# Kernel optimization log

Hardware: AMD Instinct MI355X
Metric: run time of the kernel (lower is better)

Reference implementation:

```python
import jax, jax.numpy as jnp
import numpy as np

B, R, N, F = 8, 8, 1024, 256


def setup_inputs() -> dict:
    key = jax.random.key(0)
    k1, k2 = jax.random.split(key)
    inputs = jax.random.normal(k1, (B, R, N, F), dtype=jnp.float32)
    Bs = jax.random.normal(k2, (R, F, F), dtype=jnp.float32) * 0.05
    return {"inputs": inputs, "Bs": Bs}


def reference(inputs, Bs):
    # E_r @ B_r : [B,R,N,F] x [R,F,F] -> [B,R,N,F]
    e = jnp.einsum("brnf,rfg->brng", inputs, Bs)
    # (E_r B_r) @ E_r^T : [B,R,N,F] x [B,R,M,F] -> [B,R,N,M]
    scores = jnp.einsum("brng,brmg->brnm", e, inputs)
    return jax.nn.sigmoid(scores)
```

## Files before the change

### kernel.cpp

```cpp
#include <hip/hip_runtime.h>


typedef float   f32x4 __attribute__((ext_vector_type(4)));
typedef _Float16 f16x8 __attribute__((ext_vector_type(8)));

#define WS_E_OFF   0
#define WS_BST_OFF 16777216
#define WS_e_OFF   17301504

__global__ __launch_bounds__(256) void bl_convert(
    const float* __restrict__ E, const float* __restrict__ Bs,
    _Float16* __restrict__ wsE, _Float16* __restrict__ wsBsT) {
  int bid = blockIdx.x, tid = threadIdx.x;
  if (bid < 8192) {
    int cid = (bid << 8) + tid;
    int br  = cid >> 15;
    int rem = cid & 32767;
    int fc  = rem >> 10;
    int n   = rem & 1023;
    const float* src = E + ((size_t)br << 18) + n * 256 + (fc << 3);
    f32x4 v0 = *(const f32x4*)src;
    f32x4 v1 = *(const f32x4*)(src + 4);
    f16x8 h;
    h[0] = (_Float16)v0[0]; h[1] = (_Float16)v0[1];
    h[2] = (_Float16)v0[2]; h[3] = (_Float16)v0[3];
    h[4] = (_Float16)v1[0]; h[5] = (_Float16)v1[1];
    h[6] = (_Float16)v1[2]; h[7] = (_Float16)v1[3];
    *(f16x8*)(wsE + ((size_t)br << 18) + (fc << 13) + (n << 3)) = h;
  } else {
    int cid = ((bid - 8192) << 8) + tid;
    int r   = cid >> 13;
    int rem = cid & 8191;
    int fc  = rem >> 8;
    int g   = rem & 255;
    const float* src = Bs + (r << 16) + (fc << 3) * 256 + g;
    f16x8 h;
#pragma unroll
    for (int j = 0; j < 8; ++j) h[j] = (_Float16)src[j * 256];
    *(f16x8*)(wsBsT + (r << 16) + (fc << 11) + (g << 3)) = h;
  }
}

__global__ __launch_bounds__(256) void bl_gemm1(
    const _Float16* __restrict__ wsE, const _Float16* __restrict__ wsBsT,
    _Float16* __restrict__ wse) {
  __shared__ _Float16 sA[8192];
  __shared__ _Float16 sB[8192];
  int bid = blockIdx.x;
  int br = bid >> 4;
  int t  = bid & 15;
  int n0 = (t >> 1) << 7;
  int g0 = (t & 1) << 7;
  int r  = br & 7;
  int tid  = threadIdx.x;
  int lane = tid & 63, wave = tid >> 6;
  int wm = wave >> 1, wn = wave & 1;
  int quad = lane >> 4, l16 = lane & 15;

  const _Float16* aG = wsE   + ((size_t)br << 18) + (n0 << 3);
  const _Float16* bG = wsBsT + (r << 16) + (g0 << 3);

  f32x4 acc[4][4] = {};

  for (int kk = 0; kk < 4; ++kk) {
    __syncthreads();
#pragma unroll
    for (int i = 0; i < 4; ++i) {
      int c = (i << 8) + tid;
      int kcl = c >> 7, nl = c & 127;
      *(f16x8*)&sA[c << 3] = *(const f16x8*)(aG + (((kk << 3) + kcl) << 13) + (nl << 3));
    }
#pragma unroll
    for (int i = 0; i < 4; ++i) {
      int c = (i << 8) + tid;
      int kcl = c >> 7, gl = c & 127;
      *(f16x8*)&sB[c << 3] = *(const f16x8*)(bG + (((kk << 3) + kcl) << 11) + (gl << 3));
    }
    __syncthreads();
#pragma unroll
    for (int ks = 0; ks < 2; ++ks) {
      int kc = (ks << 2) + quad;
      f16x8 af[4], bf[4];
#pragma unroll
      for (int rt = 0; rt < 4; ++rt)
        af[rt] = *(const f16x8*)&sA[((kc << 7) + (wm << 6) + (rt << 4) + l16) << 3];
#pragma unroll
      for (int ct = 0; ct < 4; ++ct)
        bf[ct] = *(const f16x8*)&sB[((kc << 7) + (wn << 6) + (ct << 4) + l16) << 3];
#pragma unroll
      for (int rt = 0; rt < 4; ++rt)
#pragma unroll
        for (int ct = 0; ct < 4; ++ct)
          acc[rt][ct] = __builtin_amdgcn_mfma_f32_16x16x32_f16(af[rt], bf[ct], acc[rt][ct], 0, 0, 0);
    }
  }
  _Float16* eB = wse + ((size_t)br << 18);
#pragma unroll
  for (int rt = 0; rt < 4; ++rt) {
#pragma unroll
    for (int ct = 0; ct < 4; ++ct) {
      int g  = g0 + (wn << 6) + (ct << 4) + l16;
      int gc = g >> 3, gj = g & 7;
#pragma unroll
      for (int i = 0; i < 4; ++i) {
        int n = n0 + (wm << 6) + (rt << 4) + (quad << 2) + i;
        eB[(gc << 13) + (n << 3) + gj] = (_Float16)acc[rt][ct][i];
      }
    }
  }
}

__global__ __launch_bounds__(256) void bl_gemm2(
    const _Float16* __restrict__ wse, const _Float16* __restrict__ wsE,
    float* __restrict__ out) {
  __shared__ _Float16 sA[8192];
  __shared__ _Float16 sB[8192];
  int bid = blockIdx.x;
  int br = bid >> 6;
  int t  = bid & 63;
  int n0 = (t >> 3) << 7;
  int m0 = (t & 7) << 7;
  int tid  = threadIdx.x;
  int lane = tid & 63, wave = tid >> 6;
  int wm = wave >> 1, wn = wave & 1;
  int quad = lane >> 4, l16 = lane & 15;

  const _Float16* aG = wse + ((size_t)br << 18) + (n0 << 3);
  const _Float16* bG = wsE + ((size_t)br << 18) + (m0 << 3);

  f32x4 acc[4][4] = {};

  for (int kk = 0; kk < 4; ++kk) {
    __syncthreads();
#pragma unroll
    for (int i = 0; i < 4; ++i) {
      int c = (i << 8) + tid;
      int kcl = c >> 7, nl = c & 127;
      *(f16x8*)&sA[c << 3] = *(const f16x8*)(aG + (((kk << 3) + kcl) << 13) + (nl << 3));
    }
#pragma unroll
    for (int i = 0; i < 4; ++i) {
      int c = (i << 8) + tid;
      int kcl = c >> 7, ml = c & 127;
      *(f16x8*)&sB[c << 3] = *(const f16x8*)(bG + (((kk << 3) + kcl) << 13) + (ml << 3));
    }
    __syncthreads();
#pragma unroll
    for (int ks = 0; ks < 2; ++ks) {
      int kc = (ks << 2) + quad;
      f16x8 af[4], bf[4];
#pragma unroll
      for (int rt = 0; rt < 4; ++rt)
        af[rt] = *(const f16x8*)&sA[((kc << 7) + (wm << 6) + (rt << 4) + l16) << 3];
#pragma unroll
      for (int ct = 0; ct < 4; ++ct)
        bf[ct] = *(const f16x8*)&sB[((kc << 7) + (wn << 6) + (ct << 4) + l16) << 3];
#pragma unroll
      for (int rt = 0; rt < 4; ++rt)
#pragma unroll
        for (int ct = 0; ct < 4; ++ct)
          acc[rt][ct] = __builtin_amdgcn_mfma_f32_16x16x32_f16(af[rt], bf[ct], acc[rt][ct], 0, 0, 0);
    }
  }
  float* oB = out + ((size_t)br << 20);
#pragma unroll
  for (int rt = 0; rt < 4; ++rt) {
#pragma unroll
    for (int ct = 0; ct < 4; ++ct) {
      int m = m0 + (wn << 6) + (ct << 4) + l16;
#pragma unroll
      for (int i = 0; i < 4; ++i) {
        int n = n0 + (wm << 6) + (rt << 4) + (quad << 2) + i;
        float x = acc[rt][ct][i];
        float s = __builtin_amdgcn_rcpf(1.0f + __expf(-x));
        oB[((size_t)n << 10) + m] = s;
      }
    }
  }
}

extern "C" void kernel_launch(void* const* d_in, const int* in_sizes, int n_in,
                              void* d_out, int out_size, void* d_ws, size_t ws_size,
                              hipStream_t stream) {
  const float* E  = (const float*)d_in[0];
  const float* Bs = (const float*)d_in[1];
  _Float16* wsE   = (_Float16*)d_ws + WS_E_OFF;
  _Float16* wsBsT = (_Float16*)d_ws + WS_BST_OFF;
  _Float16* wse   = (_Float16*)d_ws + WS_e_OFF;
  float* out = (float*)d_out;

  bl_convert<<<8448, 256, 0, stream>>>(E, Bs, wsE, wsBsT);
  bl_gemm1<<<1024, 256, 0, stream>>>(wsE, wsBsT, wse);
  bl_gemm2<<<4096, 256, 0, stream>>>(wse, wsE, out);
}
```

Baseline: 392.8 us.

## Stage convert through LDS, use direct global-to-LDS loads, nontemporal sigmoid stores

The convert kernel now transposes tiles through shared memory, so both the fp32 reads and the fp16 writes are coalesced, and the launch uses far fewer, larger blocks. Both GEMM kernels switch their tile staging to global_load_lds builtins, which write straight into LDS without passing through registers. The gemm2 epilogue precomputes a base output pointer, replaces the rcp intrinsic with a true division, and writes the fp32 output with nontemporal stores. The intent is to cut wasted memory traffic and VGPR pressure, at the cost of an exact divide and a dependence on direct-to-LDS load semantics.

```diff
diff --git a/kernel.cpp b/kernel.cpp
--- a/kernel.cpp
+++ b/kernel.cpp
@@ -1,43 +1,74 @@
 #include <hip/hip_runtime.h>
 
 
-typedef float   f32x4 __attribute__((ext_vector_type(4)));
+typedef float    f32x4 __attribute__((ext_vector_type(4)));
 typedef _Float16 f16x8 __attribute__((ext_vector_type(8)));
 
 #define WS_E_OFF   0
 #define WS_BST_OFF 16777216
 #define WS_e_OFF   17301504
 
+typedef __attribute__((address_space(3))) void  lds_void;
+typedef const __attribute__((address_space(1))) void glb_void;
+#define GLOAD16(gp, lp) __builtin_amdgcn_global_load_lds((glb_void*)(gp), (lds_void*)(lp), 16, 0, 0)
+
 __global__ __launch_bounds__(256) void bl_convert(
     const float* __restrict__ E, const float* __restrict__ Bs,
     _Float16* __restrict__ wsE, _Float16* __restrict__ wsBsT) {
-  int bid = blockIdx.x, tid = threadIdx.x;
-  if (bid < 8192) {
-    int cid = (bid << 8) + tid;
-    int br  = cid >> 15;
-    int rem = cid & 32767;
-    int fc  = rem >> 10;
-    int n   = rem & 1023;
-    const float* src = E + ((size_t)br << 18) + n * 256 + (fc << 3);
-    f32x4 v0 = *(const f32x4*)src;
-    f32x4 v1 = *(const f32x4*)(src + 4);
-    f16x8 h;
-    h[0] = (_Float16)v0[0]; h[1] = (_Float16)v0[1];
-    h[2] = (_Float16)v0[2]; h[3] = (_Float16)v0[3];
-    h[4] = (_Float16)v1[0]; h[5] = (_Float16)v1[1];
-    h[6] = (_Float16)v1[2]; h[7] = (_Float16)v1[3];
-    *(f16x8*)(wsE + ((size_t)br << 18) + (fc << 13) + (n << 3)) = h;
+  __shared__ _Float16 s[16640];
+  int bid = blockIdx.x, t = threadIdx.x;
+  if (bid < 1024) {
+    int br = bid >> 4, n0 = (bid & 15) << 6;
+    const float* src = E + ((size_t)br << 18) + ((size_t)n0 << 8);
+#pragma unroll
+    for (int i = 0; i < 8; ++i) {
+      int idx = (i << 8) + t;
+      int n_l = idx >> 5, fc = idx & 31;
+      const float* p = src + (n_l << 8) + (fc << 3);
+      f32x4 v0 = *(const f32x4*)p;
+      f32x4 v1 = *(const f32x4*)(p + 4);
+      f16x8 h;
+      h[0]=(_Float16)v0[0]; h[1]=(_Float16)v0[1]; h[2]=(_Float16)v0[2]; h[3]=(_Float16)v0[3];
+      h[4]=(_Float16)v1[0]; h[5]=(_Float16)v1[1]; h[6]=(_Float16)v1[2]; h[7]=(_Float16)v1[3];
+      *(f16x8*)&s[fc * 520 + (n_l << 3)] = h;
+    }
+    __syncthreads();
+    _Float16* dst = wsE + ((size_t)br << 18) + (n0 << 3);
+#pragma unroll
+    for (int i = 0; i < 8; ++i) {
+      int idx = (i << 8) + t;
+      int fc = idx >> 6, n_l = idx & 63;
+      *(f16x8*)(dst + (fc << 13) + (n_l << 3)) = *(const f16x8*)&s[fc * 520 + (n_l << 3)];
+    }
   } else {
-    int cid = ((bid - 8192) << 8) + tid;
-    int r   = cid >> 13;
-    int rem = cid & 8191;
-    int fc  = rem >> 8;
-    int g   = rem & 255;
-    const float* src = Bs + (r << 16) + (fc << 3) * 256 + g;
-    f16x8 h;
-#pragma unroll
-    for (int j = 0; j < 8; ++j) h[j] = (_Float16)src[j * 256];
-    *(f16x8*)(wsBsT + (r << 16) + (fc << 11) + (g << 3)) = h;
+    int b2 = bid - 1024;
+    int r = b2 >> 2, f0 = (b2 & 3) << 6;
+    const float* src = Bs + (r << 16) + (f0 << 8);
+#pragma unroll
+    for (int i = 0; i < 8; ++i) {
+      int idx = (i << 8) + t;
+      int f_l = idx >> 5, gc8 = idx & 31;
+      const float* p = src + (f_l << 8) + (gc8 << 3);
+      f32x4 v0 = *(const f32x4*)p;
+      f32x4 v1 = *(const f32x4*)(p + 4);
+      int base = (f_l >> 3) * 2056 + (gc8 << 6) + (f_l & 7);
+      s[base +  0] = (_Float16)v0[0];
+      s[base +  8] = (_Float16)v0[1];
+      s[base + 16] = (_Float16)v0[2];
+      s[base + 24] = (_Float16)v0[3];
+      s[base + 32] = (_Float16)v1[0];
+      s[base + 40] = (_Float16)v1[1];
+      s[base + 48] = (_Float16)v1[2];
+      s[base + 56] = (_Float16)v1[3];
+    }
+    __syncthreads();
+    _Float16* dst = wsBsT + (r << 16) + (f0 << 8);
+#pragma unroll
+    for (int i = 0; i < 8; ++i) {
+      int idx = (i << 8) + t;
+      int fc_l = idx >> 8, g = idx & 255;
+      *(f16x8*)(dst + (fc_l << 11) + (g << 3)) = *(const f16x8*)&s[fc_l * 2056 + (g << 3)];
+    }
   }
 }
 
@@ -67,14 +98,12 @@
 #pragma unroll
     for (int i = 0; i < 4; ++i) {
       int c = (i << 8) + tid;
-      int kcl = c >> 7, nl = c & 127;
-      *(f16x8*)&sA[c << 3] = *(const f16x8*)(aG + (((kk << 3) + kcl) << 13) + (nl << 3));
-    }
-#pragma unroll
-    for (int i = 0; i < 4; ++i) {
-      int c = (i << 8) + tid;
-      int kcl = c >> 7, gl = c & 127;
-      *(f16x8*)&sB[c << 3] = *(const f16x8*)(bG + (((kk << 3) + kcl) << 11) + (gl << 3));
+      GLOAD16(aG + (((kk << 3) + (c >> 7)) << 13) + ((c & 127) << 3), &sA[c << 3]);
+    }
+#pragma unroll
+    for (int i = 0; i < 4; ++i) {
+      int c = (i << 8) + tid;
+      GLOAD16(bG + (((kk << 3) + (c >> 7)) << 11) + ((c & 127) << 3), &sB[c << 3]);
     }
     __syncthreads();
 #pragma unroll
@@ -135,14 +164,12 @@
 #pragma unroll
     for (int i = 0; i < 4; ++i) {
       int c = (i << 8) + tid;
-      int kcl = c >> 7, nl = c & 127;
-      *(f16x8*)&sA[c << 3] = *(const f16x8*)(aG + (((kk << 3) + kcl) << 13) + (nl << 3));
-    }
-#pragma unroll
-    for (int i = 0; i < 4; ++i) {
-      int c = (i << 8) + tid;
-      int kcl = c >> 7, ml = c & 127;
-      *(f16x8*)&sB[c << 3] = *(const f16x8*)(bG + (((kk << 3) + kcl) << 13) + (ml << 3));
+      GLOAD16(aG + (((kk << 3) + (c >> 7)) << 13) + ((c & 127) << 3), &sA[c << 3]);
+    }
+#pragma unroll
+    for (int i = 0; i < 4; ++i) {
+      int c = (i << 8) + tid;
+      GLOAD16(bG + (((kk << 3) + (c >> 7)) << 13) + ((c & 127) << 3), &sB[c << 3]);
     }
     __syncthreads();
 #pragma unroll
@@ -162,18 +189,18 @@
           acc[rt][ct] = __builtin_amdgcn_mfma_f32_16x16x32_f16(af[rt], bf[ct], acc[rt][ct], 0, 0, 0);
     }
   }
-  float* oB = out + ((size_t)br << 20);
+  float* p0 = out + ((size_t)br << 20)
+            + ((size_t)(n0 + (wm << 6) + (quad << 2)) << 10)
+            + m0 + (wn << 6) + l16;
 #pragma unroll
   for (int rt = 0; rt < 4; ++rt) {
 #pragma unroll
     for (int ct = 0; ct < 4; ++ct) {
-      int m = m0 + (wn << 6) + (ct << 4) + l16;
 #pragma unroll
       for (int i = 0; i < 4; ++i) {
-        int n = n0 + (wm << 6) + (rt << 4) + (quad << 2) + i;
         float x = acc[rt][ct][i];
-        float s = __builtin_amdgcn_rcpf(1.0f + __expf(-x));
-        oB[((size_t)n << 10) + m] = s;
+        float sg = 1.0f / (1.0f + __expf(-x));
+        __builtin_nontemporal_store(sg, p0 + (rt << 14) + (i << 10) + (ct << 4));
       }
     }
   }
@@ -189,7 +216,7 @@
   _Float16* wse   = (_Float16*)d_ws + WS_e_OFF;
   float* out = (float*)d_out;
 
-  bl_convert<<<8448, 256, 0, stream>>>(E, Bs, wsE, wsBsT);
+  bl_convert<<<1056, 256, 0, stream>>>(E, Bs, wsE, wsBsT);
   bl_gemm1<<<1024, 256, 0, stream>>>(wsE, wsBsT, wse);
   bl_gemm2<<<4096, 256, 0, stream>>>(wse, wsE, out);
 }
```

Measured after the change: 406.2 us. 3.4% more time.
